# Kernel optimization log

Measured on AMD Instinct MI355X. Metric: run time of the kernel, lower is better.

Reference implementation:

```python
import jax, jax.numpy as jnp
import numpy as np

NUM_STEPS = 100
STEP = 2.0 / (NUM_STEPS - 1)          # bin width over [-1, 1]
EPS = 1.0 / NUM_STEPS
TSIZE = NUM_STEPS                      # bin centers t_k = -1 + k*STEP, k=0..99
B, D = 4096, 128
NUM_CLASSES = 100


def setup_inputs() -> dict:
    key = jax.random.key(0)
    k1, k2 = jax.random.split(key)
    embeddings = jax.random.normal(k1, (B, D), dtype=jnp.float32)
    classes = jax.random.randint(k2, (B,), 0, NUM_CLASSES)
    return {"embeddings": embeddings, "classes": classes}


def _histogram_loss(embeddings, classes):
    n = embeddings.shape[0]
    iu, ju = np.triu_indices(n, 1)            # static upper-triangular pair indices
    # cosine similarity of all pairs (outer_cosine_similarity)
    en = embeddings / jnp.linalg.norm(embeddings, axis=1, keepdims=True)
    dists = en @ en.T                          # [B, B]
    s = jnp.clip(dists[iu, ju], -1.0 + 1e-6, 1.0 - 1e-6)   # [P]
    pos = (classes[iu] == classes[ju])         # [P] bool

    # soft triangular-kernel 2-bin scatter (equivalent to indsa/indsb masking):
    # bin j gets (t_j + STEP - s)/STEP, bin j+1 gets (s - t_j)/STEP
    j = jnp.floor((s + 1.0 - 1e-6) / STEP).astype(jnp.int32)   # lower bin index
    t_j = j.astype(s.dtype) * STEP - 1.0
    w_hi = (s - t_j) / STEP                    # weight for bin j+1
    w_lo = (t_j + STEP - s) / STEP             # weight for bin j

    def histogram(mask):
        m = mask.astype(s.dtype)
        size = m.sum()
        h = jnp.zeros((TSIZE,), dtype=s.dtype)
        h = h.at[j].add(w_lo * m).at[j + 1].add(w_hi * m)
        return h / size

    hist_pos = histogram(pos)
    hist_neg = histogram(~pos)
    # tril-masked repeat + sum(0) in the original is exactly a cumulative sum
    hist_pos_cdf = jnp.cumsum(hist_pos)
    return jnp.sum(hist_neg * hist_pos_cdf)


def reference(embeddings, classes):
    return _histogram_loss(embeddings, classes)
```

## Files before the change

### kernel.cpp

```cpp
#include <hip/hip_runtime.h>
#include <hip/hip_bf16.h>
#include <cstddef>

#define BN 4096
#define DD 128
#define NSTEPS 100
#define PTILE 128
#define PLSTR 136
#define GRID_T (BN / PTILE)
#define NOFF 496
#define NBLK2 512
#define NREPC 16

typedef __attribute__((ext_vector_type(8))) short bf16x8;
typedef __attribute__((ext_vector_type(4))) float f32x4;

__device__ __forceinline__ void faddf(float* p, float v) { unsafeAtomicAdd(p, v); }

#define ZERON 166

__global__ __launch_bounds__(256) void hl_normalize(const float* __restrict__ emb,
                                                    ushort* __restrict__ out,
                                                    float* __restrict__ zero_blk) {
    if (blockIdx.x == 0 && threadIdx.x < ZERON) zero_blk[threadIdx.x] = 0.f;
    int w = threadIdx.x >> 6;
    int lane = threadIdx.x & 63;
    int row = (blockIdx.x << 2) + w;
    const float2 v = *(const float2*)(emb + (size_t)row * DD + 2 * lane);
    float ss = v.x * v.x + v.y * v.y;
    #pragma unroll
    for (int off = 32; off > 0; off >>= 1) ss += __shfl_xor(ss, off);
    float inv = 1.0f / sqrtf(ss);
    __hip_bfloat16 b0 = __float2bfloat16(v.x * inv);
    __hip_bfloat16 b1 = __float2bfloat16(v.y * inv);
    ushort2 pk;
    pk.x = *(ushort*)&b0;
    pk.y = *(ushort*)&b1;
    *(ushort2*)(out + (size_t)row * DD + 2 * lane) = pk;
}

__global__ __launch_bounds__(256) void hl_poscls(const ushort* __restrict__ nemb,
                                                 const int* __restrict__ cls,
                                                 float* __restrict__ gPos,
                                                 unsigned int* __restrict__ gDoneP,
                                                 float* __restrict__ gCdf) {
    const int c = blockIdx.x;
    __shared__ int idx[256];
    __shared__ int scan[256];
    __shared__ ushort As[64 * PLSTR];
    __shared__ ushort Bs[64 * PLSTR];
    __shared__ float hpos[NREPC * 101];
    __shared__ int mTot;
    __shared__ int lastFlag;
    const int tid = threadIdx.x;

    for (int i = tid; i < NREPC * 101; i += 256) hpos[i] = 0.f;

    const int base = tid * 16;
    int myCnt = 0;
    #pragma unroll
    for (int k = 0; k < 16; ++k) myCnt += (cls[base + k] == c);
    scan[tid] = myCnt;
    __syncthreads();
    for (int s = 1; s < 256; s <<= 1) {
        int v = (tid >= s) ? scan[tid - s] : 0;
        __syncthreads();
        scan[tid] += v;
        __syncthreads();
    }
    int w = scan[tid] - myCnt;
    if (tid == 255) mTot = scan[255] > 256 ? 256 : scan[255];
    #pragma unroll
    for (int k = 0; k < 16; ++k) {
        if (cls[base + k] == c && w < 256) { idx[w] = base + k; ++w; }
    }
    __syncthreads();
    const int m = mTot;
    const int nt = (m + 63) >> 6;

    constexpr float STEPF = 2.0f / 99.0f;
    constexpr float INVSTEP = 49.5f;
    constexpr float CLIPV = 1.0f - 1e-6f;

    const int lane = tid & 63;
    const int wv = tid >> 6;
    const int lr = lane & 15;
    const int kg = lane >> 4;
    const int rep = (lane & 15) * 101;

    for (int si = 0; si < nt; ++si) {
        for (int sj = si; sj < nt; ++sj) {
            __syncthreads();
            #pragma unroll
            for (int it = 0; it < 4; ++it) {
                int q = it * 256 + tid;
                int row = q >> 4;
                int ch = q & 15;
                int ga = si * 64 + row;
                int gb = sj * 64 + row;
                int ra = idx[ga < m ? ga : 0];
                int rb = idx[gb < m ? gb : 0];
                *(float4*)(&As[row * PLSTR + ch * 8]) =
                    *(const float4*)(nemb + (size_t)ra * DD + ch * 8);
                *(float4*)(&Bs[row * PLSTR + ch * 8]) =
                    *(const float4*)(nemb + (size_t)rb * DD + ch * 8);
            }
            __syncthreads();

            f32x4 zero4 = {0.f, 0.f, 0.f, 0.f};
            f32x4 pacc[4] = {zero4, zero4, zero4, zero4};
            #pragma unroll
            for (int ks = 0; ks < 4; ++ks) {
                bf16x8 af = *(const bf16x8*)(&As[(wv * 16 + lr) * PLSTR + ks * 32 + kg * 8]);
                #pragma unroll
                for (int fb = 0; fb < 4; ++fb) {
                    bf16x8 bf = *(const bf16x8*)(&Bs[(fb * 16 + lr) * PLSTR + ks * 32 + kg * 8]);
                    pacc[fb] = __builtin_amdgcn_mfma_f32_16x16x32_bf16(af, bf, pacc[fb], 0, 0, 0);
                }
            }

            #pragma unroll
            for (int fb = 0; fb < 4; ++fb) {
                const int gb = sj * 64 + fb * 16 + lr;
                #pragma unroll
                for (int j = 0; j < 4; ++j) {
                    const int ga = si * 64 + wv * 16 + kg * 4 + j;
                    if (ga < gb && gb < m) {
                        float s = pacc[fb][j];
                        s = fminf(fmaxf(s, -CLIPV), CLIPV);
                        float u = (s + CLIPV) * INVSTEP;
                        int jb = (int)u;
                        if (jb > 98) jb = 98;
                        float t_j = (float)jb * STEPF - 1.0f;
                        float w_hi = (s - t_j) * INVSTEP;
                        float w_lo = 1.0f - w_hi;
                        faddf(&hpos[rep + jb], w_lo);
                        faddf(&hpos[rep + jb + 1], w_hi);
                    }
                }
            }
        }
    }
    __syncthreads();
    if (tid < NSTEPS) {
        float v = 0.f;
        #pragma unroll
        for (int r = 0; r < NREPC; ++r) v += hpos[r * 101 + tid];
        if (v != 0.f) faddf(&gPos[tid], v);
    }
    __threadfence();
    if (tid == 0) {
        unsigned int tk = atomicAdd(gDoneP, 1u);
        lastFlag = (tk == NSTEPS - 1);
    }
    __syncthreads();
    if (lastFlag) {
        float v = (tid < NSTEPS)
            ? __hip_atomic_load(&gPos[tid], __ATOMIC_RELAXED, __HIP_MEMORY_SCOPE_AGENT) : 0.f;
        if (tid < 128) hpos[tid] = v;
        __syncthreads();
        for (int off = 1; off < 128; off <<= 1) {
            float x = 0.f;
            if (tid < 128 && tid >= off) x = hpos[tid - off];
            __syncthreads();
            if (tid < 128) hpos[tid] += x;
            __syncthreads();
        }
        const float invsp = 1.0f / hpos[NSTEPS - 1];
        if (tid < NSTEPS) gCdf[tid] = hpos[tid] * invsp;
    }
}

__global__ __launch_bounds__(256, 2) void hl_neg(const ushort* __restrict__ nemb,
                                                 const int* __restrict__ cls,
                                                 const float* __restrict__ gCdf,
                                                 float* __restrict__ gLoss,
                                                 float* __restrict__ gCnt,
                                                 unsigned int* __restrict__ gDone,
                                                 float* __restrict__ out) {
    __shared__ ushort As[PTILE * 128];
    __shared__ ushort Bs[PTILE * 128];
    __shared__ float cdfL[NREPC * 101];
    __shared__ float red[8];
    __shared__ int clsA[PTILE], clsB[PTILE];

    const int tid = threadIdx.x;
    const int lane = tid & 63;
    const int wid = tid >> 6;
    const int wr = wid >> 1, wc = wid & 1;
    const int lr = lane & 15;
    const int kg = lane >> 4;

    int ti0, tj0, ti1 = 0, nu = 1;
    {
        int t = blockIdx.x;
        if (t < NOFF) {
            int ti = 0, rem = t;
            while (rem >= GRID_T - 1 - ti) { rem -= GRID_T - 1 - ti; ++ti; }
            ti0 = ti; tj0 = ti + 1 + rem;
        } else {
            int d = (t - NOFF) * 2;
            ti0 = tj0 = d; ti1 = d + 1; nu = 2;
        }
    }

    for (int i = tid; i < NREPC * NSTEPS; i += 256) {
        int r = i / NSTEPS, b = i - r * NSTEPS;
        cdfL[r * 101 + b] = gCdf[b];
    }

    constexpr float STEPF = 2.0f / 99.0f;
    constexpr float INVSTEP = 49.5f;
    constexpr float CLIPV = 1.0f - 1e-6f;
    const float* crep = &cdfL[(lane & 15) * 101];
    const int li_base = wr * 64 + (kg << 2);
    const int lj_base = wc * 64 + lr;

    float lacc = 0.f, lcnt = 0.f;
    const int rloc = lane >> 4;
    const int pch = lane & 15;

    for (int u = 0; u < nu; ++u) {
        const int ti = u ? ti1 : ti0;
        const int tj = u ? ti1 : tj0;
        const bool diag = (ti == tj);

        __syncthreads();
        if (tid < PTILE) clsA[tid] = cls[ti * PTILE + tid];
        else             clsB[tid - PTILE] = cls[tj * PTILE + (tid - PTILE)];

        {
            const ushort* Ag = nemb + (size_t)(ti * PTILE) * DD;
            const ushort* Bg = nemb + (size_t)(tj * PTILE) * DD;
            #pragma unroll
            for (int t = 0; t < 8; ++t) {
                int row = wid * 32 + t * 4 + rloc;
                int lch = pch ^ (row & 7);
                const ushort* ga = Ag + (size_t)row * DD + lch * 8;
                ushort* la = &As[(wid * 32 + t * 4) * 128];
                __builtin_amdgcn_global_load_lds(
                    (const __attribute__((address_space(1))) void*)ga,
                    (__attribute__((address_space(3))) void*)la, 16, 0, 0);
            }
            if (!diag) {
                #pragma unroll
                for (int t = 0; t < 8; ++t) {
                    int row = wid * 32 + t * 4 + rloc;
                    int lch = pch ^ (row & 7);
                    const ushort* gb = Bg + (size_t)row * DD + lch * 8;
                    ushort* lb = &Bs[(wid * 32 + t * 4) * 128];
                    __builtin_amdgcn_global_load_lds(
                        (const __attribute__((address_space(1))) void*)gb,
                        (__attribute__((address_space(3))) void*)lb, 16, 0, 0);
                }
            }
        }
        __syncthreads();

        const ushort* Bsel = diag ? As : Bs;
        const int* clsBsel = diag ? clsA : clsB;

        f32x4 zero4 = {0.f, 0.f, 0.f, 0.f};
        f32x4 acc[4][4];
        #pragma unroll
        for (int a = 0; a < 4; ++a)
            #pragma unroll
            for (int b = 0; b < 4; ++b) acc[a][b] = zero4;

        #pragma unroll
        for (int ks = 0; ks < 4; ++ks) {
            bf16x8 af[4], bfr[4];
            #pragma unroll
            for (int f = 0; f < 4; ++f) {
                int arow = wr * 64 + f * 16 + lr;
                int pca = ((ks << 2) | kg) ^ (arow & 7);
                af[f] = *(const bf16x8*)(&As[arow * 128 + pca * 8]);
                int brow = wc * 64 + f * 16 + lr;
                int pcb = ((ks << 2) | kg) ^ (brow & 7);
                bfr[f] = *(const bf16x8*)(&Bsel[brow * 128 + pcb * 8]);
            }
            #pragma unroll
            for (int fa = 0; fa < 4; ++fa)
                #pragma unroll
                for (int fb = 0; fb < 4; ++fb)
                    acc[fa][fb] = __builtin_amdgcn_mfma_f32_16x16x32_bf16(af[fa], bfr[fb], acc[fa][fb], 0, 0, 0);
        }

        int ca[16];
        #pragma unroll
        for (int fa = 0; fa < 4; ++fa)
            #pragma unroll
            for (int j = 0; j < 4; ++j) ca[fa * 4 + j] = clsA[li_base + fa * 16 + j];

        const bool offdiag = !diag;
        #pragma unroll
        for (int fb = 0; fb < 4; ++fb) {
            const int lj = lj_base + fb * 16;
            const int cb = clsBsel[lj];
            #pragma unroll
            for (int fa = 0; fa < 4; ++fa) {
                const int li0 = li_base + fa * 16;
                f32x4 v = acc[fa][fb];
                #pragma unroll
                for (int j = 0; j < 4; ++j) {
                    const int li = li0 + j;
                    const bool mneg = (offdiag || (li < lj)) && (ca[fa * 4 + j] != cb);
                    float s = v[j];
                    s = fminf(fmaxf(s, -CLIPV), CLIPV);
                    float uu = (s + CLIPV) * INVSTEP;
                    int jb = (int)uu;
                    if (jb > 98) jb = 98;
                    float t_j = (float)jb * STEPF - 1.0f;
                    float w_hi = (s - t_j) * INVSTEP;
                    float w_lo = 1.0f - w_hi;
                    float c0 = crep[jb];
                    float c1 = crep[jb + 1];
                    float mm = mneg ? 1.0f : 0.0f;
                    lacc = fmaf(mm, fmaf(w_lo, c0, w_hi * c1), lacc);
                    lcnt += mm;
                }
            }
        }
    }

    #pragma unroll
    for (int off = 32; off > 0; off >>= 1) {
        lacc += __shfl_xor(lacc, off);
        lcnt += __shfl_xor(lcnt, off);
    }
    if (lane == 0) { red[wid] = lacc; red[4 + wid] = lcnt; }
    __syncthreads();
    if (tid == 0) {
        float L = red[0] + red[1] + red[2] + red[3];
        float C = red[4] + red[5] + red[6] + red[7];
        faddf(&gLoss[blockIdx.x & 31], L);
        faddf(&gCnt[blockIdx.x & 31], C);
        __threadfence();
        unsigned int tk = atomicAdd(gDone, 1u);
        if (tk == NBLK2 - 1) {
            __threadfence();
            float ls = 0.f, cs = 0.f;
            for (int i = 0; i < 32; ++i) {
                ls += __hip_atomic_load(&gLoss[i], __ATOMIC_RELAXED, __HIP_MEMORY_SCOPE_AGENT);
                cs += __hip_atomic_load(&gCnt[i], __ATOMIC_RELAXED, __HIP_MEMORY_SCOPE_AGENT);
            }
            out[0] = ls / cs;
        }
    }
}

extern "C" void kernel_launch(void* const* d_in, const int* in_sizes, int n_in,
                              void* d_out, int out_size, void* d_ws, size_t ws_size,
                              hipStream_t stream) {
    const float* emb = (const float*)d_in[0];
    const int* classes = (const int*)d_in[1];
    float* out = (float*)d_out;

    ushort* nemb = (ushort*)d_ws;
    float* ctl = (float*)((char*)d_ws + (size_t)BN * DD * sizeof(ushort));
    float* gPos = ctl;
    float* gLoss = gPos + NSTEPS;
    float* gCnt = gLoss + 32;
    unsigned int* gDone = (unsigned int*)(gCnt + 32);
    unsigned int* gDoneP = gDone + 1;
    float* gCdf = (float*)(gDoneP + 1);

    hl_normalize<<<BN / 4, 256, 0, stream>>>(emb, nemb, ctl);
    hl_poscls<<<NSTEPS, 256, 0, stream>>>(nemb, classes, gPos, gDoneP, gCdf);
    hl_neg<<<NBLK2, 256, 0, stream>>>(nemb, classes, gCdf, gLoss, gCnt, gDone, out);
}
```

Before: 46.34 us.

## Spill MFMA accumulators to LDS and rework bin lookup with packed CDF pairs

The negative-pair kernel now writes its 64 accumulator values to a shared arena that aliases the A/B tiles, then processes them in a non-unrolled loop. This is meant to cut register pressure and code size in the epilogue. The CDF table becomes float2 pairs (value, delta) with 8 replicas, so each pair needs one LDS load and one FMA. The bin weight is computed as the fractional part of u in both kernels. The cost is an extra LDS round trip, two more barriers and a serialized loop, with small floating-point differences in the weights.

```diff
diff --git a/kernel.cpp b/kernel.cpp
--- a/kernel.cpp
+++ b/kernel.cpp
@@ -7,10 +7,11 @@
 #define NSTEPS 100
 #define PTILE 128
 #define PLSTR 136
-#define GRID_T (BN / PTILE)
+#define GRID_T 32
 #define NOFF 496
 #define NBLK2 512
-#define NREPC 16
+#define NREPH 16
+#define NREPC2 8
 
 typedef __attribute__((ext_vector_type(8))) short bf16x8;
 typedef __attribute__((ext_vector_type(4))) float f32x4;
@@ -49,12 +50,12 @@
     __shared__ int scan[256];
     __shared__ ushort As[64 * PLSTR];
     __shared__ ushort Bs[64 * PLSTR];
-    __shared__ float hpos[NREPC * 101];
+    __shared__ float hpos[NREPH * 101];
     __shared__ int mTot;
     __shared__ int lastFlag;
     const int tid = threadIdx.x;
 
-    for (int i = tid; i < NREPC * 101; i += 256) hpos[i] = 0.f;
+    for (int i = tid; i < NREPH * 101; i += 256) hpos[i] = 0.f;
 
     const int base = tid * 16;
     int myCnt = 0;
@@ -78,7 +79,6 @@
     const int m = mTot;
     const int nt = (m + 63) >> 6;
 
-    constexpr float STEPF = 2.0f / 99.0f;
     constexpr float INVSTEP = 49.5f;
     constexpr float CLIPV = 1.0f - 1e-6f;
 
@@ -131,8 +131,7 @@
                         float u = (s + CLIPV) * INVSTEP;
                         int jb = (int)u;
                         if (jb > 98) jb = 98;
-                        float t_j = (float)jb * STEPF - 1.0f;
-                        float w_hi = (s - t_j) * INVSTEP;
+                        float w_hi = u - (float)jb;
                         float w_lo = 1.0f - w_hi;
                         faddf(&hpos[rep + jb], w_lo);
                         faddf(&hpos[rep + jb + 1], w_hi);
@@ -145,7 +144,7 @@
     if (tid < NSTEPS) {
         float v = 0.f;
         #pragma unroll
-        for (int r = 0; r < NREPC; ++r) v += hpos[r * 101 + tid];
+        for (int r = 0; r < NREPH; ++r) v += hpos[r * 101 + tid];
         if (v != 0.f) faddf(&gPos[tid], v);
     }
     __threadfence();
@@ -178,9 +177,11 @@
                                                  float* __restrict__ gCnt,
                                                  unsigned int* __restrict__ gDone,
                                                  float* __restrict__ out) {
-    __shared__ ushort As[PTILE * 128];
-    __shared__ ushort Bs[PTILE * 128];
-    __shared__ float cdfL[NREPC * 101];
+    __shared__ __align__(16) char arena[65536];
+    ushort* As = (ushort*)arena;
+    ushort* Bs = (ushort*)(arena + 32768);
+    float* accL = (float*)arena;
+    __shared__ float2 cdf2[NREPC2 * 101];
     __shared__ float red[8];
     __shared__ int clsA[PTILE], clsB[PTILE];
 
@@ -204,15 +205,17 @@
         }
     }
 
-    for (int i = tid; i < NREPC * NSTEPS; i += 256) {
+    for (int i = tid; i < NREPC2 * NSTEPS; i += 256) {
         int r = i / NSTEPS, b = i - r * NSTEPS;
-        cdfL[r * 101 + b] = gCdf[b];
-    }
-
-    constexpr float STEPF = 2.0f / 99.0f;
+        float c0 = gCdf[b];
+        float c1 = gCdf[(b < NSTEPS - 1) ? b + 1 : NSTEPS - 1];
+        float2 cd; cd.x = c0; cd.y = c1 - c0;
+        cdf2[r * 101 + b] = cd;
+    }
+
     constexpr float INVSTEP = 49.5f;
     constexpr float CLIPV = 1.0f - 1e-6f;
-    const float* crep = &cdfL[(lane & 15) * 101];
+    const float2* crep2 = &cdf2[(lane & 7) * 101];
     const int li_base = wr * 64 + (kg << 2);
     const int lj_base = wc * 64 + lr;
 
@@ -286,40 +289,36 @@
                     acc[fa][fb] = __builtin_amdgcn_mfma_f32_16x16x32_bf16(af[fa], bfr[fb], acc[fa][fb], 0, 0, 0);
         }
 
-        int ca[16];
+        __syncthreads();
+
         #pragma unroll
-        for (int fa = 0; fa < 4; ++fa)
-            #pragma unroll
-            for (int j = 0; j < 4; ++j) ca[fa * 4 + j] = clsA[li_base + fa * 16 + j];
+        for (int fb = 0; fb < 4; ++fb)
+            #pragma unroll
+            for (int fa = 0; fa < 4; ++fa)
+                #pragma unroll
+                for (int j = 0; j < 4; ++j)
+                    accL[(fb * 16 + fa * 4 + j) * 256 + tid] = acc[fa][fb][j];
+        __syncthreads();
 
         const bool offdiag = !diag;
-        #pragma unroll
-        for (int fb = 0; fb < 4; ++fb) {
+        #pragma unroll 1
+        for (int p = 0; p < 64; ++p) {
+            const int fb = p >> 4, fa = (p >> 2) & 3, j = p & 3;
+            const int li = li_base + fa * 16 + j;
             const int lj = lj_base + fb * 16;
-            const int cb = clsBsel[lj];
-            #pragma unroll
-            for (int fa = 0; fa < 4; ++fa) {
-                const int li0 = li_base + fa * 16;
-                f32x4 v = acc[fa][fb];
-                #pragma unroll
-                for (int j = 0; j < 4; ++j) {
-                    const int li = li0 + j;
-                    const bool mneg = (offdiag || (li < lj)) && (ca[fa * 4 + j] != cb);
-                    float s = v[j];
-                    s = fminf(fmaxf(s, -CLIPV), CLIPV);
-                    float uu = (s + CLIPV) * INVSTEP;
-                    int jb = (int)uu;
-                    if (jb > 98) jb = 98;
-                    float t_j = (float)jb * STEPF - 1.0f;
-                    float w_hi = (s - t_j) * INVSTEP;
-                    float w_lo = 1.0f - w_hi;
-                    float c0 = crep[jb];
-                    float c1 = crep[jb + 1];
-                    float mm = mneg ? 1.0f : 0.0f;
-                    lacc = fmaf(mm, fmaf(w_lo, c0, w_hi * c1), lacc);
-                    lcnt += mm;
-                }
-            }
+            float s = accL[p * 256 + tid];
+            int ca = clsA[li];
+            int cb = clsBsel[lj];
+            const bool mneg = (offdiag || (li < lj)) && (ca != cb);
+            s = fminf(fmaxf(s, -CLIPV), CLIPV);
+            float uu = (s + CLIPV) * INVSTEP;
+            int jb = (int)uu;
+            if (jb > 98) jb = 98;
+            float w_hi = uu - (float)jb;
+            float2 cd = crep2[jb];
+            float mm = mneg ? 1.0f : 0.0f;
+            lacc = fmaf(mm, fmaf(w_hi, cd.y, cd.x), lacc);
+            lcnt += mm;
         }
     }
 
```

Result: slower. 51.64 us (+11.4%).
